# Kernel tuning notes

Measured on AMD Instinct MI355X. Metric: run time of the kernel, lower is better.

## Reference

```python
import jax, jax.numpy as jnp
import numpy as np

N = 50000      # nodes
E = 800000     # edges
F_IN = 128     # input_channels
H = 128        # hidden_channels
OUT = 10       # output_channels
G = 64         # graphs in batch


def setup_inputs() -> dict:
    key = jax.random.key(0)
    ks = jax.random.split(key, 16)
    s = 0.05
    inp = {
        "x": jax.random.normal(ks[0], (N, F_IN), jnp.float32),
        "edge_index": jax.random.randint(ks[1], (2, E), 0, N, jnp.int64 if jax.config.jax_enable_x64 else jnp.int32),
        "batch": jnp.sort(jax.random.randint(ks[2], (N,), 0, G, jnp.int32)),
        "conv1_w": jax.random.normal(ks[3], (F_IN, H), jnp.float32) * s,
        "conv1_b": jnp.zeros((H,), jnp.float32),
        "conv2_w": jax.random.normal(ks[4], (H, H), jnp.float32) * s,
        "conv2_b": jnp.zeros((H,), jnp.float32),
        "conv3_w": jax.random.normal(ks[5], (H, H), jnp.float32) * s,
        "conv3_b": jnp.zeros((H,), jnp.float32),
        "fc1_w": jax.random.normal(ks[6], (H, 8 * H), jnp.float32) * s,
        "fc1_b": jnp.zeros((8 * H,), jnp.float32),
        "fc2_w": jax.random.normal(ks[7], (8 * H, 4 * H), jnp.float32) * s,
        "fc2_b": jnp.zeros((4 * H,), jnp.float32),
        "fc3_w": jax.random.normal(ks[8], (4 * H, 2 * H), jnp.float32) * s,
        "fc3_b": jnp.zeros((2 * H,), jnp.float32),
        "fc4_w": jax.random.normal(ks[9], (2 * H, H), jnp.float32) * s,
        "fc4_b": jnp.zeros((H,), jnp.float32),
        "fc5_w": jax.random.normal(ks[10], (H, OUT), jnp.float32) * s,
        "fc5_b": jnp.zeros((OUT,), jnp.float32),
    }
    return inp


def _gcn_conv(x, w, b, src, dst, norm, n_nodes):
    # GCNConv: out = D^{-1/2} (A + I) D^{-1/2} X W + b   (self-loops already in src/dst)
    xw = x @ w                                        # [N, H]
    msg = xw[src] * norm[:, None]                     # gather + scale, [E+N, H]
    return jax.ops.segment_sum(msg, dst, num_segments=n_nodes) + b


def reference(x, edge_index, batch,
              conv1_w, conv1_b, conv2_w, conv2_b, conv3_w, conv3_b,
              fc1_w, fc1_b, fc2_w, fc2_b, fc3_w, fc3_b,
              fc4_w, fc4_b, fc5_w, fc5_b):
    n = x.shape[0]
    loop = jnp.arange(n, dtype=edge_index.dtype)
    src = jnp.concatenate([edge_index[0], loop])      # add self-loops
    dst = jnp.concatenate([edge_index[1], loop])
    deg = jax.ops.segment_sum(jnp.ones_like(dst, dtype=x.dtype), dst, num_segments=n)
    dinv = jnp.where(deg > 0, jax.lax.rsqrt(deg), 0.0)
    norm = dinv[src] * dinv[dst]                      # symmetric normalization per edge

    h = jax.nn.relu(_gcn_conv(x, conv1_w, conv1_b, src, dst, norm, n))
    h = jax.nn.relu(_gcn_conv(h, conv2_w, conv2_b, src, dst, norm, n))
    h = _gcn_conv(h, conv3_w, conv3_b, src, dst, norm, n)

    # global mean pool over graphs
    sums = jax.ops.segment_sum(h, batch, num_segments=G)
    cnt = jax.ops.segment_sum(jnp.ones((n,), x.dtype), batch, num_segments=G)
    f = sums / jnp.maximum(cnt, 1.0)[:, None]         # [G, H]

    y = jax.nn.relu(f @ fc1_w + fc1_b)
    y = jax.nn.relu(y @ fc2_w + fc2_b)
    y = jax.nn.relu(y @ fc3_w + fc3_b)
    y = jax.nn.relu(y @ fc4_w + fc4_b)
    # dropout p=0.5 is identity in eval mode
    y = y @ fc5_w + fc5_b                             # [G, OUT]
    return (f, y)
```

## Files before the change

kernel.cpp:

```cpp
#include <hip/hip_runtime.h>
#include <stdint.h>

#define N_NODES 50000
#define N_EDGES 800000
#define FEAT    128
#define NGRAPH  64

#define E_BLKS    3125
#define GEMM_BLKS 6250
#define GR_BLKS   (GEMM_BLKS + E_BLKS)

typedef __attribute__((ext_vector_type(8))) short short8;
typedef __attribute__((ext_vector_type(4))) float floatx4;

static __device__ __forceinline__ ushort f2bf(float f) {
  uint32_t x = __float_as_uint(f);
  x += 0x7FFF + ((x >> 16) & 1);
  return (ushort)(x >> 16);
}
static __device__ __forceinline__ float bfLo(uint32_t u) {
  return __uint_as_float(u << 16);
}
static __device__ __forceinline__ float bfHi(uint32_t u) {
  return __uint_as_float(u & 0xFFFF0000u);
}

static __device__ __forceinline__ void cvt4T(const float* __restrict__ in,
                                             ushort* __restrict__ outT, int i) {
  float4 v = ((const float4*)in)[i];
  int k = (4 * i) >> 7;
  int n = (4 * i) & 127;
  outT[(size_t)(n + 0) * FEAT + k] = f2bf(v.x);
  outT[(size_t)(n + 1) * FEAT + k] = f2bf(v.y);
  outT[(size_t)(n + 2) * FEAT + k] = f2bf(v.z);
  outT[(size_t)(n + 3) * FEAT + k] = f2bf(v.w);
}

__global__ __launch_bounds__(256) void wcvt(const float* __restrict__ w0,
                                            const float* __restrict__ w1,
                                            ushort* __restrict__ wbT) {
  int i = blockIdx.x * 256 + threadIdx.x;
  if (i < 4096) cvt4T(w0, wbT, i);
  else cvt4T(w1, wbT + FEAT * FEAT, i - 4096);
}

static __device__ __forceinline__ void gemm_body_f32a(int wave, int lane,
                                                      const float* __restrict__ X,
                                                      const ushort* __restrict__ WT,
                                                      ushort* __restrict__ XW) {
  int mt = wave >> 3;
  int nt = wave & 7;
  int m0 = mt * 16, n0 = nt * 16;
  int r = lane & 15, quad = lane >> 4;
  floatx4 acc = {0.f, 0.f, 0.f, 0.f};
  const float* xrow = X + (size_t)(m0 + r) * FEAT;
  const ushort* wrow = WT + (size_t)(n0 + r) * FEAT;
#pragma unroll
  for (int kb = 0; kb < 4; ++kb) {
    int k0 = kb * 32 + quad * 8;
    float4 f0 = *(const float4*)(xrow + k0);
    float4 f1 = *(const float4*)(xrow + k0 + 4);
    short8 a;
    a[0] = (short)f2bf(f0.x); a[1] = (short)f2bf(f0.y);
    a[2] = (short)f2bf(f0.z); a[3] = (short)f2bf(f0.w);
    a[4] = (short)f2bf(f1.x); a[5] = (short)f2bf(f1.y);
    a[6] = (short)f2bf(f1.z); a[7] = (short)f2bf(f1.w);
    short8 b = *(const short8*)(wrow + k0);
    acc = __builtin_amdgcn_mfma_f32_16x16x32_bf16(a, b, acc, 0, 0, 0);
  }
#pragma unroll
  for (int reg = 0; reg < 4; ++reg) {
    int row = quad * 4 + reg;
    XW[(size_t)(m0 + row) * FEAT + n0 + r] = f2bf(acc[reg]);
  }
}

__global__ __launch_bounds__(256) void gemm_rank(const float* __restrict__ x,
                                                 const ushort* __restrict__ wbT,
                                                 ushort* __restrict__ msl,
                                                 const int* __restrict__ dst,
                                                 int* __restrict__ cnt,
                                                 int* __restrict__ rank) {
  int b = blockIdx.x, t = threadIdx.x;
  int third = b / 3;
  int rem = b - third * 3;
  if (rem < 2) {
    int gb = third * 2 + rem;
    gemm_body_f32a(gb * 4 + (t >> 6), t & 63, x, wbT, msl);
  } else {
    int e = third * 256 + t;
    rank[e] = atomicAdd(&cnt[dst[e]], 1);
  }
}

__global__ __launch_bounds__(256) void dinv_scan1(const int* __restrict__ cnt,
                                                  const int* __restrict__ batch,
                                                  float* __restrict__ dinv,
                                                  float* __restrict__ cnt_g,
                                                  int* __restrict__ ptr,
                                                  int* __restrict__ bsums) {
  __shared__ int tmp[256];
  __shared__ int bins[NGRAPH];
  if (threadIdx.x < NGRAPH) bins[threadIdx.x] = 0;
  int i = blockIdx.x * 256 + threadIdx.x;
  int v = (i < N_NODES) ? cnt[i] : 0;
  tmp[threadIdx.x] = v;
  __syncthreads();
  for (int off = 1; off < 256; off <<= 1) {
    int t = (threadIdx.x >= off) ? tmp[threadIdx.x - off] : 0;
    __syncthreads();
    tmp[threadIdx.x] += t;
    __syncthreads();
  }
  if (i < N_NODES) ptr[i] = tmp[threadIdx.x] - v;
  if (threadIdx.x == 255) bsums[blockIdx.x] = tmp[255];
  if (i < N_NODES) {
    dinv[i] = rsqrtf((float)v + 1.0f);
    atomicAdd(&bins[batch[i]], 1);
  }
  __syncthreads();
  if (threadIdx.x < NGRAPH && bins[threadIdx.x] > 0)
    atomicAdd(&cnt_g[threadIdx.x], (float)bins[threadIdx.x]);
}

__global__ __launch_bounds__(256) void scan2(int* __restrict__ bsums, int nb) {
  __shared__ int tmp[256];
  int v = (threadIdx.x < nb) ? bsums[threadIdx.x] : 0;
  tmp[threadIdx.x] = v;
  __syncthreads();
  for (int off = 1; off < 256; off <<= 1) {
    int t = (threadIdx.x >= off) ? tmp[threadIdx.x - off] : 0;
    __syncthreads();
    tmp[threadIdx.x] += t;
    __syncthreads();
  }
  if (threadIdx.x < nb) bsums[threadIdx.x] = tmp[threadIdx.x] - v;
}

__global__ __launch_bounds__(256) void scan3(int* __restrict__ ptr,
                                             const int* __restrict__ bsums) {
  int i = blockIdx.x * 256 + threadIdx.x;
  if (i < N_NODES) ptr[i] += bsums[blockIdx.x];
}

__global__ __launch_bounds__(256) void fill_csr(const int* __restrict__ src,
                                                const int* __restrict__ dst,
                                                const int* __restrict__ rank,
                                                const int* __restrict__ ptr,
                                                const float* __restrict__ dinv,
                                                int2* __restrict__ edges) {
  int e = blockIdx.x * 256 + threadIdx.x;
  if (e >= N_EDGES) return;
  int s = src[e];
  edges[ptr[dst[e]] + rank[e]] = make_int2(s, __float_as_int(dinv[s]));
}

__global__ __launch_bounds__(256) void gemm128(const ushort* __restrict__ X,
                                               const ushort* __restrict__ WT,
                                               ushort* __restrict__ XW) {
  int wave = (blockIdx.x * 256 + threadIdx.x) >> 6;
  int lane = threadIdx.x & 63;
  int mt = wave >> 3;
  int nt = wave & 7;
  int m0 = mt * 16, n0 = nt * 16;
  int r = lane & 15, quad = lane >> 4;
  floatx4 acc = {0.f, 0.f, 0.f, 0.f};
  const ushort* xrow = X + (size_t)(m0 + r) * FEAT;
  const ushort* wrow = WT + (size_t)(n0 + r) * FEAT;
#pragma unroll
  for (int kb = 0; kb < 4; ++kb) {
    int k0 = kb * 32 + quad * 8;
    short8 a = *(const short8*)(xrow + k0);
    short8 b = *(const short8*)(wrow + k0);
    acc = __builtin_amdgcn_mfma_f32_16x16x32_bf16(a, b, acc, 0, 0, 0);
  }
#pragma unroll
  for (int reg = 0; reg < 4; ++reg) {
    int row = quad * 4 + reg;
    XW[(size_t)(m0 + row) * FEAT + n0 + r] = f2bf(acc[reg]);
  }
}

template <int MODE>
__global__ __launch_bounds__(256) void agg_kernel(const ushort* __restrict__ msg,
                                                  const float* __restrict__ dinv,
                                                  const int* __restrict__ ptr,
                                                  const int* __restrict__ cnt,
                                                  const int2* __restrict__ edges,
                                                  const float* __restrict__ bias,
                                                  void* __restrict__ outp) {
  int wave = (blockIdx.x * 256 + threadIdx.x) >> 6;
  int lane = threadIdx.x & 63;
  if (wave >= N_NODES) return;
  int v = wave;
  float di = dinv[v];
  const uint32_t* m32 = (const uint32_t*)msg;
  uint32_t su = m32[(size_t)v * 64 + lane];
  float ax0 = di * bfLo(su), ay0 = di * bfHi(su);
  float ax1 = 0.f, ay1 = 0.f, ax2 = 0.f, ay2 = 0.f, ax3 = 0.f, ay3 = 0.f;
  int start = ptr[v];
  int n = cnt[v];
  int i = 0;
  if ((start & 1) && n > 0) {
    int2 e = edges[start];
    uint32_t u = m32[(size_t)e.x * 64 + lane];
    float nrm = __int_as_float(e.y);
    ax0 = fmaf(nrm, bfLo(u), ax0);
    ay0 = fmaf(nrm, bfHi(u), ay0);
    i = 1;
  }
  for (; i + 8 <= n; i += 8) {
    const int4* ep = (const int4*)(edges + start + i);
    int4 q0 = ep[0], q1 = ep[1], q2 = ep[2], q3 = ep[3];
    uint32_t u0 = m32[(size_t)q0.x * 64 + lane];
    uint32_t u1 = m32[(size_t)q0.z * 64 + lane];
    uint32_t u2 = m32[(size_t)q1.x * 64 + lane];
    uint32_t u3 = m32[(size_t)q1.z * 64 + lane];
    uint32_t u4 = m32[(size_t)q2.x * 64 + lane];
    uint32_t u5 = m32[(size_t)q2.z * 64 + lane];
    uint32_t u6 = m32[(size_t)q3.x * 64 + lane];
    uint32_t u7 = m32[(size_t)q3.z * 64 + lane];
    float n0 = __int_as_float(q0.y), n1 = __int_as_float(q0.w);
    float n2 = __int_as_float(q1.y), n3 = __int_as_float(q1.w);
    float n4 = __int_as_float(q2.y), n5 = __int_as_float(q2.w);
    float n6 = __int_as_float(q3.y), n7 = __int_as_float(q3.w);
    ax0 = fmaf(n0, bfLo(u0), ax0); ay0 = fmaf(n0, bfHi(u0), ay0);
    ax1 = fmaf(n1, bfLo(u1), ax1); ay1 = fmaf(n1, bfHi(u1), ay1);
    ax2 = fmaf(n2, bfLo(u2), ax2); ay2 = fmaf(n2, bfHi(u2), ay2);
    ax3 = fmaf(n3, bfLo(u3), ax3); ay3 = fmaf(n3, bfHi(u3), ay3);
    ax0 = fmaf(n4, bfLo(u4), ax0); ay0 = fmaf(n4, bfHi(u4), ay0);
    ax1 = fmaf(n5, bfLo(u5), ax1); ay1 = fmaf(n5, bfHi(u5), ay1);
    ax2 = fmaf(n6, bfLo(u6), ax2); ay2 = fmaf(n6, bfHi(u6), ay2);
    ax3 = fmaf(n7, bfLo(u7), ax3); ay3 = fmaf(n7, bfHi(u7), ay3);
  }
  for (; i < n; ++i) {
    int2 e = edges[start + i];
    float nrm = __int_as_float(e.y);
    uint32_t u = m32[(size_t)e.x * 64 + lane];
    ax0 = fmaf(nrm, bfLo(u), ax0);
    ay0 = fmaf(nrm, bfHi(u), ay0);
  }
  float ax = (ax0 + ax1) + (ax2 + ax3);
  float ay = (ay0 + ay1) + (ay2 + ay3);
  if (MODE == 2) {
    ((float2*)outp)[(size_t)v * 64 + lane] = make_float2(ax * di, ay * di);
  } else {
    ax = fmaf(ax, di, bias[2 * lane]);
    ay = fmaf(ay, di, bias[2 * lane + 1]);
    ax = fmaxf(ax, 0.f);
    ay = fmaxf(ay, 0.f);
    ushort2 h2;
    h2.x = f2bf(ax);
    h2.y = f2bf(ay);
    ((ushort2*)outp)[(size_t)v * 64 + lane] = h2;
  }
}

__global__ __launch_bounds__(256) void pool_sum(const float* __restrict__ a3,
                                                const int* __restrict__ batch,
                                                float* __restrict__ P) {
  int wave = blockIdx.x * 4 + (threadIdx.x >> 6);
  int lane = threadIdx.x & 63;
  int v0 = wave * 16;
  if (v0 >= N_NODES) return;
  int vend = v0 + 16;
  if (vend > N_NODES) vend = N_NODES;
  const float2* a2 = (const float2*)a3;
  float ax = 0.f, ay = 0.f;
  int g = batch[v0];
  for (int v = v0; v < vend; ++v) {
    int gv = batch[v];
    if (gv != g) {
      atomicAdd(&P[(size_t)g * FEAT + 2 * lane], ax);
      atomicAdd(&P[(size_t)g * FEAT + 2 * lane + 1], ay);
      ax = 0.f; ay = 0.f; g = gv;
    }
    float2 t = a2[(size_t)v * 64 + lane];
    ax += t.x;
    ay += t.y;
  }
  atomicAdd(&P[(size_t)g * FEAT + 2 * lane], ax);
  atomicAdd(&P[(size_t)g * FEAT + 2 * lane + 1], ay);
}

__device__ __forceinline__ void head_layer(const float* __restrict__ IN,
                                           float* __restrict__ OUT,
                                           const float* __restrict__ w,
                                           const float* __restrict__ b,
                                           int K, int C, int Cp, int relu,
                                           float* __restrict__ gout, int t) {
  int parts = 1024 / Cp;
  int part = t / Cp;
  int c = t - part * Cp;
  int kchunk = K / parts;
  if (t < C) OUT[t] = b[t];
  __syncthreads();
  if (c < C) {
    int k0 = part * kchunk;
    float a0 = 0.f, a1 = 0.f, a2 = 0.f, a3 = 0.f;
    const float* wp = w + (size_t)k0 * C + c;
    if ((kchunk & 3) == 0) {
#pragma unroll 4
      for (int k = 0; k < kchunk; k += 4) {
        a0 = fmaf(IN[k0 + k],     wp[(size_t)k * C],       a0);
        a1 = fmaf(IN[k0 + k + 1], wp[(size_t)(k + 1) * C], a1);
        a2 = fmaf(IN[k0 + k + 2], wp[(size_t)(k + 2) * C], a2);
        a3 = fmaf(IN[k0 + k + 3], wp[(size_t)(k + 3) * C], a3);
      }
    } else {
      for (int k = 0; k < kchunk; ++k)
        a0 = fmaf(IN[k0 + k], wp[(size_t)k * C], a0);
    }
    atomicAdd(&OUT[c], (a0 + a1) + (a2 + a3));
  }
  __syncthreads();
  if (t < C) {
    float v = OUT[t];
    if (relu) { v = fmaxf(v, 0.f); OUT[t] = v; }
    if (gout) gout[t] = v;
  }
  __syncthreads();
}

__global__ __launch_bounds__(1024) void fc_head(const float* __restrict__ P,
                                                const float* __restrict__ cnt_g,
                                                const float* __restrict__ w3,
                                                const float* __restrict__ b3,
                                                const float* __restrict__ w1,
                                                const float* __restrict__ b1,
                                                const float* __restrict__ w2,
                                                const float* __restrict__ b2,
                                                const float* __restrict__ wf3,
                                                const float* __restrict__ bf3,
                                                const float* __restrict__ w4,
                                                const float* __restrict__ b4,
                                                const float* __restrict__ w5,
                                                const float* __restrict__ b5,
                                                float* __restrict__ out_f,
                                                float* __restrict__ out_y) {
  __shared__ float A[1024];
  __shared__ float B[1024];
  int r = blockIdx.x, t = threadIdx.x;
  if (t < FEAT) A[t] = P[r * FEAT + t] / fmaxf(cnt_g[r], 1.0f);
  __syncthreads();
  head_layer(A, B, w3, b3, 128, 128, 128, 0, out_f + (size_t)r * FEAT, t);
  head_layer(B, A, w1, b1, 128, 1024, 1024, 1, nullptr, t);
  head_layer(A, B, w2, b2, 1024, 512, 512, 1, nullptr, t);
  head_layer(B, A, wf3, bf3, 512, 256, 256, 1, nullptr, t);
  head_layer(A, B, w4, b4, 256, 128, 128, 1, nullptr, t);
  head_layer(B, A, w5, b5, 128, 10, 16, 0, out_y + (size_t)r * 10, t);
}

extern "C" void kernel_launch(void* const* d_in, const int* in_sizes, int n_in,
                              void* d_out, int out_size, void* d_ws, size_t ws_size,
                              hipStream_t stream) {
  const float* x         = (const float*)d_in[0];
  const int*   ei        = (const int*)d_in[1];
  const int*   batch     = (const int*)d_in[2];
  const float* conv_w[3] = {(const float*)d_in[3], (const float*)d_in[5], (const float*)d_in[7]};
  const float* conv_b[3] = {(const float*)d_in[4], (const float*)d_in[6], (const float*)d_in[8]};
  const float* fc_w[5]   = {(const float*)d_in[9],  (const float*)d_in[11],
                            (const float*)d_in[13], (const float*)d_in[15],
                            (const float*)d_in[17]};
  const float* fc_b[5]   = {(const float*)d_in[10], (const float*)d_in[12],
                            (const float*)d_in[14], (const float*)d_in[16],
                            (const float*)d_in[18]};
  const int* e_src = ei;
  const int* e_dst = ei + N_EDGES;
  float* out_f = (float*)d_out;
  float* out_y = (float*)d_out + NGRAPH * FEAT;

  char* p = (char*)d_ws;
  auto carve = [&](size_t bytes) {
    char* r = p;
    p += (bytes + 255) & ~(size_t)255;
    return r;
  };
  int*    cnt_i   = (int*)carve(N_NODES * 4);
  float*  dinv    = (float*)carve(N_NODES * 4);
  int*    csr_ptr = (int*)carve(N_NODES * 4);
  int*    bsums   = (int*)carve(256 * 4);
  int2*   edges   = (int2*)carve((size_t)N_EDGES * 8);
  ushort* wbT     = (ushort*)carve((size_t)2 * FEAT * FEAT * 2);
  ushort* hbuf    = (ushort*)carve((size_t)N_NODES * FEAT * 2);
  float*  f_sum   = (float*)carve(NGRAPH * FEAT * 4);
  float*  cnt_g   = (float*)carve(NGRAPH * 4);
  char*   region  = carve((size_t)N_NODES * FEAT * 4);
  int*    rank    = (int*)region;
  ushort* msl     = (ushort*)(region + (size_t)N_EDGES * 4);
  float*  a3      = (float*)region;

  const int BLK_N = (N_NODES + 255) / 256;

  hipMemsetAsync(cnt_i, 0, N_NODES * 4, stream);
  hipMemsetAsync(f_sum, 0, NGRAPH * FEAT * 4 + 256, stream);

  wcvt<<<32, 256, 0, stream>>>(conv_w[0], conv_w[1], wbT);

  gemm_rank<<<GR_BLKS, 256, 0, stream>>>(x, wbT, msl, e_dst, cnt_i, rank);

  dinv_scan1<<<BLK_N, 256, 0, stream>>>(cnt_i, batch, dinv, cnt_g, csr_ptr, bsums);
  scan2<<<1, 256, 0, stream>>>(bsums, BLK_N);
  scan3<<<BLK_N, 256, 0, stream>>>(csr_ptr, bsums);

  fill_csr<<<E_BLKS, 256, 0, stream>>>(e_src, e_dst, rank, csr_ptr, dinv, edges);

  const int AGG_BLKS  = (N_NODES + 3) / 4;
  const int POOL_BLKS = (N_NODES / 16 + 3) / 4 + 1;

  agg_kernel<0><<<AGG_BLKS, 256, 0, stream>>>(msl, dinv, csr_ptr, cnt_i, edges,
                                              conv_b[0], hbuf);
  gemm128<<<GEMM_BLKS, 256, 0, stream>>>(hbuf, wbT + FEAT * FEAT, msl);
  agg_kernel<0><<<AGG_BLKS, 256, 0, stream>>>(msl, dinv, csr_ptr, cnt_i, edges,
                                              conv_b[1], hbuf);
  agg_kernel<2><<<AGG_BLKS, 256, 0, stream>>>(hbuf, dinv, csr_ptr, cnt_i, edges,
                                              nullptr, a3);
  pool_sum<<<POOL_BLKS, 256, 0, stream>>>(a3, batch, f_sum);

  fc_head<<<NGRAPH, 1024, 0, stream>>>(f_sum, cnt_g, conv_w[2], conv_b[2],
                                       fc_w[0], fc_b[0], fc_w[1], fc_b[1],
                                       fc_w[2], fc_b[2], fc_w[3], fc_b[3],
                                       fc_w[4], fc_b[4], out_f, out_y);
}
```

Before: 373.5 us.

## Split fused FC head into per-layer batched kernels with split-K atomics

Replaces the single 64-block fc_head kernel, where each block ran one graph through all layers, with six separate fc_layer launches. Each launch processes four graphs per block across column groups and splits K across blocks with atomic accumulation. ReLU is applied to inputs on load and the mean-pool division is folded into the first layer. The aim is to spread the head's weight reads across many more CUs instead of 64 blocks each re-reading every weight matrix. The cost is five extra launches, an extra memset, and global intermediate buffers.

```diff
diff --git a/kernel.cpp b/kernel.cpp
--- a/kernel.cpp
+++ b/kernel.cpp
@@ -283,72 +283,58 @@
   atomicAdd(&P[(size_t)g * FEAT + 2 * lane + 1], ay);
 }
 
-__device__ __forceinline__ void head_layer(const float* __restrict__ IN,
-                                           float* __restrict__ OUT,
-                                           const float* __restrict__ w,
-                                           const float* __restrict__ b,
-                                           int K, int C, int Cp, int relu,
-                                           float* __restrict__ gout, int t) {
-  int parts = 1024 / Cp;
-  int part = t / Cp;
-  int c = t - part * Cp;
-  int kchunk = K / parts;
-  if (t < C) OUT[t] = b[t];
-  __syncthreads();
-  if (c < C) {
-    int k0 = part * kchunk;
-    float a0 = 0.f, a1 = 0.f, a2 = 0.f, a3 = 0.f;
-    const float* wp = w + (size_t)k0 * C + c;
-    if ((kchunk & 3) == 0) {
-#pragma unroll 4
-      for (int k = 0; k < kchunk; k += 4) {
-        a0 = fmaf(IN[k0 + k],     wp[(size_t)k * C],       a0);
-        a1 = fmaf(IN[k0 + k + 1], wp[(size_t)(k + 1) * C], a1);
-        a2 = fmaf(IN[k0 + k + 2], wp[(size_t)(k + 2) * C], a2);
-        a3 = fmaf(IN[k0 + k + 3], wp[(size_t)(k + 3) * C], a3);
-      }
-    } else {
-      for (int k = 0; k < kchunk; ++k)
-        a0 = fmaf(IN[k0 + k], wp[(size_t)k * C], a0);
+template <int K, int C, int KSLICE, int RELU_IN, int DIVC, int NSPLIT>
+__global__ __launch_bounds__(256) void fc_layer(const float* __restrict__ IN,
+                                                const float* __restrict__ W,
+                                                const float* __restrict__ Bs,
+                                                const float* __restrict__ cntg,
+                                                float* __restrict__ OUT) {
+  constexpr int CB = (C + 63) / 64;
+  int lane = threadIdx.x & 63;
+  int gq = threadIdx.x >> 6;
+  int bid = blockIdx.x;
+  int kp = bid % NSPLIT;
+  int rest = bid / NSPLIT;
+  int cg = rest % CB;
+  int g = (rest / CB) * 4 + gq;
+  int c = cg * 64 + lane;
+  if (c >= C) return;
+  int k0 = kp * KSLICE;
+  const float* wp = W + (size_t)k0 * C + c;
+  const float* in = IN + (size_t)g * K + k0;
+  float cf = 1.f;
+  if (DIVC) cf = fmaxf(cntg[g], 1.f);
+  float a0 = 0.f, a1 = 0.f, a2 = 0.f, a3 = 0.f;
+  float a4 = 0.f, a5 = 0.f, a6 = 0.f, a7 = 0.f;
+#pragma unroll 2
+  for (int k = 0; k < KSLICE; k += 8) {
+    float i0 = in[k + 0], i1 = in[k + 1], i2 = in[k + 2], i3 = in[k + 3];
+    float i4 = in[k + 4], i5 = in[k + 5], i6 = in[k + 6], i7 = in[k + 7];
+    if (RELU_IN) {
+      i0 = fmaxf(i0, 0.f); i1 = fmaxf(i1, 0.f);
+      i2 = fmaxf(i2, 0.f); i3 = fmaxf(i3, 0.f);
+      i4 = fmaxf(i4, 0.f); i5 = fmaxf(i5, 0.f);
+      i6 = fmaxf(i6, 0.f); i7 = fmaxf(i7, 0.f);
     }
-    atomicAdd(&OUT[c], (a0 + a1) + (a2 + a3));
-  }
-  __syncthreads();
-  if (t < C) {
-    float v = OUT[t];
-    if (relu) { v = fmaxf(v, 0.f); OUT[t] = v; }
-    if (gout) gout[t] = v;
-  }
-  __syncthreads();
-}
-
-__global__ __launch_bounds__(1024) void fc_head(const float* __restrict__ P,
-                                                const float* __restrict__ cnt_g,
-                                                const float* __restrict__ w3,
-                                                const float* __restrict__ b3,
-                                                const float* __restrict__ w1,
-                                                const float* __restrict__ b1,
-                                                const float* __restrict__ w2,
-                                                const float* __restrict__ b2,
-                                                const float* __restrict__ wf3,
-                                                const float* __restrict__ bf3,
-                                                const float* __restrict__ w4,
-                                                const float* __restrict__ b4,
-                                                const float* __restrict__ w5,
-                                                const float* __restrict__ b5,
-                                                float* __restrict__ out_f,
-                                                float* __restrict__ out_y) {
-  __shared__ float A[1024];
-  __shared__ float B[1024];
-  int r = blockIdx.x, t = threadIdx.x;
-  if (t < FEAT) A[t] = P[r * FEAT + t] / fmaxf(cnt_g[r], 1.0f);
-  __syncthreads();
-  head_layer(A, B, w3, b3, 128, 128, 128, 0, out_f + (size_t)r * FEAT, t);
-  head_layer(B, A, w1, b1, 128, 1024, 1024, 1, nullptr, t);
-  head_layer(A, B, w2, b2, 1024, 512, 512, 1, nullptr, t);
-  head_layer(B, A, wf3, bf3, 512, 256, 256, 1, nullptr, t);
-  head_layer(A, B, w4, b4, 256, 128, 128, 1, nullptr, t);
-  head_layer(B, A, w5, b5, 128, 10, 16, 0, out_y + (size_t)r * 10, t);
+    if (DIVC) {
+      i0 /= cf; i1 /= cf; i2 /= cf; i3 /= cf;
+      i4 /= cf; i5 /= cf; i6 /= cf; i7 /= cf;
+    }
+    a0 = fmaf(i0, wp[(size_t)(k + 0) * C], a0);
+    a1 = fmaf(i1, wp[(size_t)(k + 1) * C], a1);
+    a2 = fmaf(i2, wp[(size_t)(k + 2) * C], a2);
+    a3 = fmaf(i3, wp[(size_t)(k + 3) * C], a3);
+    a4 = fmaf(i4, wp[(size_t)(k + 4) * C], a4);
+    a5 = fmaf(i5, wp[(size_t)(k + 5) * C], a5);
+    a6 = fmaf(i6, wp[(size_t)(k + 6) * C], a6);
+    a7 = fmaf(i7, wp[(size_t)(k + 7) * C], a7);
+  }
+  float s = ((a0 + a1) + (a2 + a3)) + ((a4 + a5) + (a6 + a7));
+  if (NSPLIT == 1) {
+    OUT[(size_t)g * C + c] = s + Bs[c];
+  } else {
+    atomicAdd(&OUT[(size_t)g * C + c], s + (kp == 0 ? Bs[c] : 0.f));
+  }
 }
 
 extern "C" void kernel_launch(void* const* d_in, const int* in_sizes, int n_in,
@@ -385,6 +371,10 @@
   ushort* hbuf    = (ushort*)carve((size_t)N_NODES * FEAT * 2);
   float*  f_sum   = (float*)carve(NGRAPH * FEAT * 4);
   float*  cnt_g   = (float*)carve(NGRAPH * 4);
+  float*  Y1      = (float*)carve(NGRAPH * 1024 * 4);
+  float*  Y2      = (float*)carve(NGRAPH * 512 * 4);
+  float*  Y3      = (float*)carve(NGRAPH * 256 * 4);
+  float*  Y4      = (float*)carve(NGRAPH * 128 * 4);
   char*   region  = carve((size_t)N_NODES * FEAT * 4);
   int*    rank    = (int*)region;
   ushort* msl     = (ushort*)(region + (size_t)N_EDGES * 4);
@@ -394,6 +384,7 @@
 
   hipMemsetAsync(cnt_i, 0, N_NODES * 4, stream);
   hipMemsetAsync(f_sum, 0, NGRAPH * FEAT * 4 + 256, stream);
+  hipMemsetAsync(Y2, 0, NGRAPH * (512 + 256 + 128) * 4, stream);
 
   wcvt<<<32, 256, 0, stream>>>(conv_w[0], conv_w[1], wbT);
 
@@ -417,8 +408,10 @@
                                               nullptr, a3);
   pool_sum<<<POOL_BLKS, 256, 0, stream>>>(a3, batch, f_sum);
 
-  fc_head<<<NGRAPH, 1024, 0, stream>>>(f_sum, cnt_g, conv_w[2], conv_b[2],
-                                       fc_w[0], fc_b[0], fc_w[1], fc_b[1],
-                                       fc_w[2], fc_b[2], fc_w[3], fc_b[3],
-                                       fc_w[4], fc_b[4], out_f, out_y);
-}
+  fc_layer< 128, 128, 128, 0, 1, 1><<< 32, 256, 0, stream>>>(f_sum, conv_w[2], conv_b[2], cnt_g, out_f);
+  fc_layer< 128,1024, 128, 0, 0, 1><<<256, 256, 0, stream>>>(out_f, fc_w[0], fc_b[0], nullptr, Y1);
+  fc_layer<1024, 512, 256, 1, 0, 4><<<512, 256, 0, stream>>>(Y1, fc_w[1], fc_b[1], nullptr, Y2);
+  fc_layer< 512, 256, 128, 1, 0, 4><<<256, 256, 0, stream>>>(Y2, fc_w[2], fc_b[2], nullptr, Y3);
+  fc_layer< 256, 128,  32, 1, 0, 8><<<256, 256, 0, stream>>>(Y3, fc_w[3], fc_b[3], nullptr, Y4);
+  fc_layer< 128,  10, 128, 1, 0, 1><<< 16, 256, 0, stream>>>(Y4, fc_w[4], fc_b[4], nullptr, out_y);
+}
```

After: 375.0 us. Within noise of the previous version (+0.4%).
